# Kernel optimization log

Hardware: AMD Instinct MI355X
Metric: run time of the kernel (lower is better)

The kernel has to match this reference:

```python
import jax, jax.numpy as jnp
import numpy as np
import math

B, T, C, H = 8, 1024, 1024, 16
HS = C // H  # head size 64
FF = 4 * C
EPS = 1e-5


def quant_weight(W, e, b):
    """Fake-quant with straight-through rounding, per QLinear.forward.
    W:[...,out,in], e:[...,out,1], b:[...,out,1] -> effective weight 2**e * round_ste(clip(2**-e * W))."""
    b_rel = jax.nn.relu(b)
    mn = jnp.where(b_rel > 0, -(2.0 ** (b_rel - 1)), 0.0)
    mx = jnp.where(b_rel > 0, 2.0 ** (b_rel - 1) - 1.0, 0.0)
    qw = jnp.clip((2.0 ** (-e)) * W, mn, mx)
    w = qw + jax.lax.stop_gradient(jnp.round(qw) - qw)  # STE round
    return (2.0 ** e) * w


def layer_norm(x, g, beta):
    mu = jnp.mean(x, axis=-1, keepdims=True)
    var = jnp.mean((x - mu) ** 2, axis=-1, keepdims=True)
    return (x - mu) * jax.lax.rsqrt(var + EPS) * g + beta


def _uniform(key, shape, fan_in):
    s = 1.0 / math.sqrt(fan_in)
    return jax.random.uniform(key, shape, jnp.float32, -s, s)


def setup_inputs() -> dict:
    key = jax.random.key(0)
    ks = jax.random.split(key, 8)
    d = {"x": jax.random.normal(ks[0], (B, T, C), jnp.float32)}
    # stacked per-head QKV QLinear params (bias=False)
    d["Wq"] = _uniform(ks[1], (H, HS, C), C)
    d["Wk"] = _uniform(ks[2], (H, HS, C), C)
    d["Wv"] = _uniform(ks[3], (H, HS, C), C)
    for n in ("q", "k", "v"):
        d["e" + n] = jnp.full((H, HS, 1), -8.0, jnp.float32)
        d["b" + n] = jnp.full((H, HS, 1), 32.0, jnp.float32)
    # output projection QLinear (bias=True)
    d["Wp"] = _uniform(ks[4], (C, C), C)
    d["ep"] = jnp.full((C, 1), -8.0, jnp.float32)
    d["bp"] = jnp.full((C, 1), 32.0, jnp.float32)
    d["biasp"] = jnp.zeros((C,), jnp.float32)
    # FFN QLinears
    d["W1"] = _uniform(ks[5], (FF, C), C)
    d["e1"] = jnp.full((FF, 1), -8.0, jnp.float32)
    d["b1"] = jnp.full((FF, 1), 32.0, jnp.float32)
    d["bias1"] = jnp.zeros((FF,), jnp.float32)
    d["W2"] = _uniform(ks[6], (C, FF), FF)
    d["e2"] = jnp.full((C, 1), -8.0, jnp.float32)
    d["b2"] = jnp.full((C, 1), 32.0, jnp.float32)
    d["bias2"] = jnp.zeros((C,), jnp.float32)
    # LayerNorms
    d["g1"] = jnp.ones((C,), jnp.float32)
    d["be1"] = jnp.zeros((C,), jnp.float32)
    d["g2"] = jnp.ones((C,), jnp.float32)
    d["be2"] = jnp.zeros((C,), jnp.float32)
    return d


def block_forward(x, Wq, eq, bq, Wk, ek, bk, Wv, ev, bv,
                  Wp, ep, bp, biasp, W1, e1, b1, bias1, W2, e2, b2, bias2,
                  g1, be1, g2, be2):
    h = layer_norm(x, g1, be1)
    q = jnp.einsum('btc,hdc->bhtd', h, quant_weight(Wq, eq, bq))
    k = jnp.einsum('btc,hdc->bhtd', h, quant_weight(Wk, ek, bk))
    v = jnp.einsum('btc,hdc->bhtd', h, quant_weight(Wv, ev, bv))
    # NOTE: source scales by C**-0.5 where C = n_embd (not head_size)
    wei = jnp.einsum('bhtd,bhsd->bhts', q, k) * (C ** -0.5)
    causal = jnp.tril(jnp.ones((T, T), bool))
    wei = jnp.where(causal, wei, -jnp.inf)
    wei = jax.nn.softmax(wei, axis=-1)
    att = jnp.einsum('bhts,bhsd->bhtd', wei, v)  # [B,H,T,HS]
    att = att.transpose(0, 2, 1, 3).reshape(B, T, C)  # concat heads
    x = x + att @ quant_weight(Wp, ep, bp).T + biasp
    h2 = layer_norm(x, g2, be2)
    f = jax.nn.relu(h2 @ quant_weight(W1, e1, b1).T + bias1)
    f = f @ quant_weight(W2, e2, b2).T + bias2
    return x + f


def reference(x, Wq, eq, bq, Wk, ek, bk, Wv, ev, bv,
              Wp, ep, bp, biasp, W1, e1, b1, bias1, W2, e2, b2, bias2,
              g1, be1, g2, be2):
    return block_forward(x, Wq, eq, bq, Wk, ek, bk, Wv, ev, bv,
                         Wp, ep, bp, biasp, W1, e1, b1, bias1, W2, e2, b2, bias2,
                         g1, be1, g2, be2)
```

## Files before the change

kernel.cpp:

```cpp
#include <hip/hip_runtime.h>
#include <hip/hip_bf16.h>
#include <math.h>

#define DEVI __device__ __forceinline__

typedef __attribute__((ext_vector_type(8))) short bf16x8;
typedef __attribute__((ext_vector_type(4))) float f32x4;

DEVI unsigned short f2bf(float f) {
    union { float f; unsigned u; } v; v.f = f;
    unsigned r = v.u + 0x7FFFu + ((v.u >> 16) & 1u);
    return (unsigned short)(r >> 16);
}

DEVI void gload16(const void* g, void* l) {
    __builtin_amdgcn_global_load_lds((const __attribute__((address_space(1))) void*)g,
                                     (__attribute__((address_space(3))) void*)l, 16, 0, 0);
}

#define WAITVM8() asm volatile("s_waitcnt vmcnt(8)" ::: "memory")
#define WAITVM0() asm volatile("s_waitcnt vmcnt(0)" ::: "memory")
#define WAITLG0() asm volatile("s_waitcnt lgkmcnt(0)" ::: "memory")

__global__ __launch_bounds__(256) void quant6_kernel(
    const float* __restrict__ Wq, const float* __restrict__ Wk, const float* __restrict__ Wv,
    const float* __restrict__ Wp, const float* __restrict__ W1, const float* __restrict__ W2,
    const float* __restrict__ eq, const float* __restrict__ ek, const float* __restrict__ ev,
    const float* __restrict__ ep, const float* __restrict__ e1, const float* __restrict__ e2,
    const float* __restrict__ bq, const float* __restrict__ bk, const float* __restrict__ bv,
    const float* __restrict__ bp, const float* __restrict__ b1, const float* __restrict__ b2,
    unsigned short* __restrict__ Wqkvq, unsigned short* __restrict__ Wpq,
    unsigned short* __restrict__ W1q, unsigned short* __restrict__ W2q)
{
    const int M1 = 1 << 20;
    const int NCH = 3 * M1;
    for (int c = blockIdx.x * blockDim.x + threadIdx.x; c < NCH; c += gridDim.x * blockDim.x) {
        int elem = c * 4;
        const float *W, *e, *b; unsigned short* o; int lgK, local;
        if (elem < M1)            { W = Wq; e = eq; b = bq; o = Wqkvq;          lgK = 10; local = elem; }
        else if (elem < 2 * M1)   { W = Wk; e = ek; b = bk; o = Wqkvq + M1;     lgK = 10; local = elem - M1; }
        else if (elem < 3 * M1)   { W = Wv; e = ev; b = bv; o = Wqkvq + 2 * M1; lgK = 10; local = elem - 2 * M1; }
        else if (elem < 4 * M1)   { W = Wp; e = ep; b = bp; o = Wpq;            lgK = 10; local = elem - 3 * M1; }
        else if (elem < 8 * M1)   { W = W1; e = e1; b = b1; o = W1q;            lgK = 10; local = elem - 4 * M1; }
        else                      { W = W2; e = e2; b = b2; o = W2q;            lgK = 12; local = elem - 8 * M1; }
        int row = local >> lgK;
        float evv = e[row], bvv = b[row];
        float br = fmaxf(bvv, 0.f);
        float mn, mx;
        if (br > 0.f) { float p = exp2f(br - 1.f); mn = -p; mx = p - 1.f; }
        else          { mn = 0.f; mx = 0.f; }
        float si = exp2f(-evv), so = exp2f(evv);
        union { float4 v4; float a[4]; } v;
        v.v4 = *(const float4*)(W + local);
        union { unsigned short u[4]; unsigned long long ll; } ot;
        #pragma unroll
        for (int j = 0; j < 4; j++) {
            float qw = fminf(fmaxf(si * v.a[j], mn), mx);
            ot.u[j] = f2bf(so * rintf(qw));
        }
        *(unsigned long long*)(o + local) = ot.ll;
    }
}

__global__ __launch_bounds__(256) void ln_kernel(
    const float* __restrict__ x, const float* __restrict__ g, const float* __restrict__ be,
    unsigned short* __restrict__ out)
{
    int row = blockIdx.x;
    union { float4 v4; float a[4]; } v;
    v.v4 = ((const float4*)(x + (size_t)row * 1024))[threadIdx.x];
    float s = v.a[0] + v.a[1] + v.a[2] + v.a[3];
    float s2 = v.a[0]*v.a[0] + v.a[1]*v.a[1] + v.a[2]*v.a[2] + v.a[3]*v.a[3];
    #pragma unroll
    for (int off = 32; off > 0; off >>= 1) { s += __shfl_down(s, off); s2 += __shfl_down(s2, off); }
    __shared__ float ps[4], ps2[4];
    int wave = threadIdx.x >> 6, lane = threadIdx.x & 63;
    if (lane == 0) { ps[wave] = s; ps2[wave] = s2; }
    __syncthreads();
    float mu = (ps[0] + ps[1] + ps[2] + ps[3]) * (1.0f / 1024.0f);
    float var = (ps2[0] + ps2[1] + ps2[2] + ps2[3]) * (1.0f / 1024.0f) - mu * mu;
    float rs = rsqrtf(var + 1e-5f);
    int c = threadIdx.x * 4;
    union { unsigned short u[4]; unsigned long long ll; } o;
    #pragma unroll
    for (int j = 0; j < 4; j++) o.u[j] = f2bf((v.a[j] - mu) * rs * g[c + j] + be[c + j]);
    *(unsigned long long*)(out + (size_t)row * 1024 + c) = o.ll;
}

#define GSTAGE(buf, kt) do { \
    _Pragma("unroll") for (int q_ = 0; q_ < 4; q_++) { \
        int idx_ = q_ * 256 + tid; int row_ = idx_ >> 3; int gs_ = (idx_ & 7) ^ (row_ & 7); \
        gload16(A  + (size_t)(brow + row_) * K + (kt) * 64 + gs_ * 8, &As[buf][idx_ * 8]); \
        gload16(Bw + (size_t)(bcol + row_) * K + (kt) * 64 + gs_ * 8, &Bs[buf][idx_ * 8]); \
    } } while (0)

template<int EP>
__global__ __launch_bounds__(256) void gemm_bt(
    const unsigned short* __restrict__ A, const unsigned short* __restrict__ Bw,
    int N, int K,
    const float* __restrict__ bias, const float* __restrict__ res,
    float* __restrict__ outf, unsigned short* __restrict__ outb)
{
    __shared__ __align__(16) unsigned short As[2][128 * 64];
    __shared__ __align__(16) unsigned short Bs[2][128 * 64];
    int tid = threadIdx.x, lane = tid & 63, wave = tid >> 6;
    int gx = gridDim.x;
    int nwg = gx * gridDim.y;
    int id = blockIdx.y * gx + blockIdx.x;
    int swz = (id & 7) * (nwg >> 3) + (id >> 3);
    int brow = (swz / gx) * 128, bcol = (swz % gx) * 128;
    int wr = wave >> 1, wc = wave & 1;
    int r = lane & 15, g4 = lane >> 4;
    f32x4 acc[4][4];
    #pragma unroll
    for (int i = 0; i < 4; i++)
        #pragma unroll
        for (int j = 0; j < 4; j++) acc[i][j] = (f32x4){0.f, 0.f, 0.f, 0.f};

    int nt = K >> 6;
    GSTAGE(0, 0);
    __syncthreads();
    int cur = 0;
    for (int t = 0; t < nt; ++t) {
        if (t + 1 < nt) { GSTAGE(cur ^ 1, t + 1); WAITVM8(); }
        else            { WAITVM0(); }
        __builtin_amdgcn_s_barrier();
        #pragma unroll
        for (int kk = 0; kk < 2; kk++) {
            bf16x8 af[4], bfr[4];
            #pragma unroll
            for (int mi = 0; mi < 4; mi++) {
                int rh = wr * 64 + mi * 16 + r;
                af[mi] = *(const bf16x8*)&As[cur][rh * 64 + (((kk * 4 + g4) ^ (rh & 7)) << 3)];
            }
            #pragma unroll
            for (int ni = 0; ni < 4; ni++) {
                int rh = wc * 64 + ni * 16 + r;
                bfr[ni] = *(const bf16x8*)&Bs[cur][rh * 64 + (((kk * 4 + g4) ^ (rh & 7)) << 3)];
            }
            #pragma unroll
            for (int mi = 0; mi < 4; mi++)
                #pragma unroll
                for (int ni = 0; ni < 4; ni++)
                    acc[mi][ni] = __builtin_amdgcn_mfma_f32_16x16x32_bf16(af[mi], bfr[ni], acc[mi][ni], 0, 0, 0);
        }
        __builtin_amdgcn_s_barrier();
        cur ^= 1;
    }

    #pragma unroll
    for (int mi = 0; mi < 4; mi++)
        #pragma unroll
        for (int ni = 0; ni < 4; ni++)
            #pragma unroll
            for (int i = 0; i < 4; i++) {
                int row = brow + wr * 64 + mi * 16 + g4 * 4 + i;
                int col = bcol + wc * 64 + ni * 16 + r;
                float v = acc[mi][ni][i];
                if (EP == 0) {
                    outb[(size_t)row * N + col] = f2bf(v);
                } else if (EP == 1) {
                    outf[(size_t)row * N + col] = v + bias[col] + res[(size_t)row * N + col];
                } else {
                    outb[(size_t)row * N + col] = f2bf(fmaxf(v + bias[col], 0.f));
                }
            }
}

__global__ __launch_bounds__(256) void attn_kernel(
    const unsigned short* __restrict__ qkv, unsigned short* __restrict__ att)
{
    __shared__ __align__(16) unsigned short Ks[2][64 * 64];
    __shared__ __align__(16) unsigned short Vt[2][64 * 64];
    __shared__ __align__(16) unsigned short Ps[64 * 64];
    int tid = threadIdx.x, lane = tid & 63, wave = tid >> 6;
    int pi = blockIdx.x;
    int bh = blockIdx.y, bb = bh >> 4, hh = bh & 15;
    int r = lane & 15, g4 = lane >> 4;
    const unsigned short* base = qkv + (size_t)bb * 1024 * 3072;
    const float SCL = 0.03125f * 1.4426950408889634f;
    int vd = tid & 63, vsb = tid >> 6;
    int prow = wave * 16 + r;
    int pswz = (r & 7) << 3;

    #pragma unroll
    for (int sub = 0; sub < 2; sub++) {
        int qi = sub ? (15 - pi) : pi;
        int q0 = qi * 64;
        int qrow = q0 + prow;

        bf16x8 qf[2];
        #pragma unroll
        for (int kk = 0; kk < 2; kk++)
            qf[kk] = *(const bf16x8*)&base[(size_t)qrow * 3072 + hh * 64 + kk * 32 + g4 * 8];

        f32x4 oacc[4];
        #pragma unroll
        for (int i = 0; i < 4; i++) oacc[i] = (f32x4){0.f, 0.f, 0.f, 0.f};
        float m_i = -INFINITY, l_i = 0.f;

        unsigned short vtmp[16];
        {
            #pragma unroll
            for (int half = 0; half < 2; half++) {
                int idx = half * 256 + tid;
                int row = idx >> 3, slot = idx & 7;
                int gs = slot ^ (row & 7);
                gload16(base + (size_t)row * 3072 + 1024 + hh * 64 + gs * 8, &Ks[0][idx * 8]);
            }
            #pragma unroll
            for (int i2 = 0; i2 < 16; i2++)
                vtmp[i2] = base[(size_t)(vsb * 16 + i2) * 3072 + 2048 + hh * 64 + vd];
            union { unsigned short u[8]; bf16x8 v; } w0, w1;
            #pragma unroll
            for (int i2 = 0; i2 < 8; i2++) { w0.u[i2] = vtmp[i2]; w1.u[i2] = vtmp[8 + i2]; }
            int s0 = (vsb * 2) ^ (vd & 7), s1 = (vsb * 2 + 1) ^ (vd & 7);
            *(bf16x8*)&Vt[0][vd * 64 + s0 * 8] = w0.v;
            *(bf16x8*)&Vt[0][vd * 64 + s1 * 8] = w1.v;
        }
        __syncthreads();

        for (int ki = 0; ki <= qi; ki++) {
            int cur = ki & 1;
            bool pre = (ki < qi);
            if (pre) {
                int k1 = (ki + 1) * 64;
                #pragma unroll
                for (int half = 0; half < 2; half++) {
                    int idx = half * 256 + tid;
                    int row = idx >> 3, slot = idx & 7;
                    int gs = slot ^ (row & 7);
                    gload16(base + (size_t)(k1 + row) * 3072 + 1024 + hh * 64 + gs * 8, &Ks[cur ^ 1][idx * 8]);
                }
                #pragma unroll
                for (int i2 = 0; i2 < 16; i2++)
                    vtmp[i2] = base[(size_t)(k1 + vsb * 16 + i2) * 3072 + 2048 + hh * 64 + vd];
            }

            int k0 = ki * 64;
            f32x4 sacc[4];
            #pragma unroll
            for (int c4 = 0; c4 < 4; c4++) sacc[c4] = (f32x4){0.f, 0.f, 0.f, 0.f};
            #pragma unroll
            for (int c4 = 0; c4 < 4; c4++) {
                int krow = c4 * 16 + r;
                #pragma unroll
                for (int kk = 0; kk < 2; kk++) {
                    int slot = (g4 + kk * 4) ^ (krow & 7);
                    bf16x8 kf = *(const bf16x8*)&Ks[cur][krow * 64 + slot * 8];
                    sacc[c4] = __builtin_amdgcn_mfma_f32_16x16x32_bf16(kf, qf[kk], sacc[c4], 0, 0, 0);
                }
            }
            bool diag = (ki == qi);
            float sv[4][4];
            float smax = -INFINITY;
            #pragma unroll
            for (int c4 = 0; c4 < 4; c4++)
                #pragma unroll
                for (int i = 0; i < 4; i++) {
                    float s = sacc[c4][i];
                    if (diag && (k0 + c4 * 16 + g4 * 4 + i) > qrow) s = -INFINITY;
                    sv[c4][i] = s;
                    smax = fmaxf(smax, s);
                }
            smax = fmaxf(smax, __shfl_xor(smax, 16));
            smax = fmaxf(smax, __shfl_xor(smax, 32));
            float mn = fmaxf(m_i, smax);
            float fs = exp2f((m_i - mn) * SCL);
            float nb = -mn * SCL;
            m_i = mn;
            float rsum = 0.f;
            float pv[4][4];
            #pragma unroll
            for (int c4 = 0; c4 < 4; c4++)
                #pragma unroll
                for (int i = 0; i < 4; i++) {
                    float p = exp2f(fmaf(sv[c4][i], SCL, nb));
                    pv[c4][i] = p;
                    rsum += p;
                }
            rsum += __shfl_xor(rsum, 16);
            rsum += __shfl_xor(rsum, 32);
            l_i = l_i * fs + rsum;
            #pragma unroll
            for (int n4 = 0; n4 < 4; n4++)
                #pragma unroll
                for (int i = 0; i < 4; i++) oacc[n4][i] *= fs;
            #pragma unroll
            for (int c4 = 0; c4 < 4; c4++) {
                union { unsigned short u[4]; unsigned long long ll; } pk;
                #pragma unroll
                for (int i = 0; i < 4; i++) pk.u[i] = f2bf(pv[c4][i]);
                int idx16 = (prow * 64 + c4 * 16 + g4 * 4) ^ pswz;
                *(unsigned long long*)&Ps[idx16] = pk.ll;
            }
            WAITLG0();
            if (pre) {
                union { unsigned short u[8]; bf16x8 v; } w0, w1;
                #pragma unroll
                for (int i2 = 0; i2 < 8; i2++) { w0.u[i2] = vtmp[i2]; w1.u[i2] = vtmp[8 + i2]; }
                int s0 = (vsb * 2) ^ (vd & 7), s1 = (vsb * 2 + 1) ^ (vd & 7);
                *(bf16x8*)&Vt[cur ^ 1][vd * 64 + s0 * 8] = w0.v;
                *(bf16x8*)&Vt[cur ^ 1][vd * 64 + s1 * 8] = w1.v;
            }
            bf16x8 pa[2];
            #pragma unroll
            for (int kk = 0; kk < 2; kk++)
                pa[kk] = *(const bf16x8*)&Ps[(prow * 64 + kk * 32 + g4 * 8) ^ pswz];
            #pragma unroll
            for (int n4 = 0; n4 < 4; n4++) {
                int d = n4 * 16 + r;
                #pragma unroll
                for (int kk = 0; kk < 2; kk++) {
                    bf16x8 vf = *(const bf16x8*)&Vt[cur][d * 64 + (((kk * 4 + g4) ^ (d & 7)) << 3)];
                    oacc[n4] = __builtin_amdgcn_mfma_f32_16x16x32_bf16(vf, pa[kk], oacc[n4], 0, 0, 0);
                }
            }
            __syncthreads();
        }

        float inv = 1.f / l_i;
        #pragma unroll
        for (int n4 = 0; n4 < 4; n4++) {
            union { unsigned short u[4]; unsigned long long ll; } ok;
            #pragma unroll
            for (int i = 0; i < 4; i++) ok.u[i] = f2bf(oacc[n4][i] * inv);
            size_t oidx = ((size_t)(bb * 1024 + qrow)) * 1024 + hh * 64 + n4 * 16 + g4 * 4;
            *(unsigned long long*)&att[oidx] = ok.ll;
        }
    }
}

extern "C" void kernel_launch(void* const* d_in, const int* in_sizes, int n_in,
                              void* d_out, int out_size, void* d_ws, size_t ws_size,
                              hipStream_t stream)
{
    const float* x     = (const float*)d_in[0];
    const float* Wq    = (const float*)d_in[1];
    const float* Wk    = (const float*)d_in[2];
    const float* Wv    = (const float*)d_in[3];
    const float* eq    = (const float*)d_in[4];
    const float* bq    = (const float*)d_in[5];
    const float* ek    = (const float*)d_in[6];
    const float* bk    = (const float*)d_in[7];
    const float* ev    = (const float*)d_in[8];
    const float* bv    = (const float*)d_in[9];
    const float* Wp    = (const float*)d_in[10];
    const float* ep    = (const float*)d_in[11];
    const float* bp    = (const float*)d_in[12];
    const float* biasp = (const float*)d_in[13];
    const float* W1    = (const float*)d_in[14];
    const float* e1    = (const float*)d_in[15];
    const float* b1    = (const float*)d_in[16];
    const float* bias1 = (const float*)d_in[17];
    const float* W2    = (const float*)d_in[18];
    const float* e2    = (const float*)d_in[19];
    const float* b2    = (const float*)d_in[20];
    const float* bias2 = (const float*)d_in[21];
    const float* g1    = (const float*)d_in[22];
    const float* be1   = (const float*)d_in[23];
    const float* g2    = (const float*)d_in[24];
    const float* be2   = (const float*)d_in[25];

    const size_t MB = 1ull << 20;
    char* ws = (char*)d_ws;
    unsigned short* Wqkvq = (unsigned short*)(ws);
    unsigned short* Wpq   = (unsigned short*)(ws + 6 * MB);
    unsigned short* W1q   = (unsigned short*)(ws + 8 * MB);
    unsigned short* W2q   = (unsigned short*)(ws + 16 * MB);
    unsigned short* hbuf  = (unsigned short*)(ws + 24 * MB);
    unsigned short* qkvb  = (unsigned short*)(ws + 40 * MB);
    unsigned short* fbuf  = qkvb;
    unsigned short* attb  = (unsigned short*)(ws + 88 * MB);
    float*          x2    = (float*)(ws + 104 * MB);

    quant6_kernel<<<2048, 256, 0, stream>>>(Wq, Wk, Wv, Wp, W1, W2,
                                            eq, ek, ev, ep, e1, e2,
                                            bq, bk, bv, bp, b1, b2,
                                            Wqkvq, Wpq, W1q, W2q);

    ln_kernel<<<8192, 256, 0, stream>>>(x, g1, be1, hbuf);
    gemm_bt<0><<<dim3(24, 64), 256, 0, stream>>>(hbuf, Wqkvq, 3072, 1024, nullptr, nullptr, nullptr, qkvb);
    attn_kernel<<<dim3(8, 128), 256, 0, stream>>>(qkvb, attb);
    gemm_bt<1><<<dim3(8, 64), 256, 0, stream>>>(attb, Wpq, 1024, 1024, biasp, x, x2, nullptr);
    ln_kernel<<<8192, 256, 0, stream>>>(x2, g2, be2, hbuf);
    gemm_bt<2><<<dim3(32, 64), 256, 0, stream>>>(hbuf, W1q, 4096, 1024, bias1, nullptr, nullptr, fbuf);
    gemm_bt<1><<<dim3(8, 64), 256, 0, stream>>>(fbuf, W2q, 1024, 4096, bias2, x2, (float*)d_out, nullptr);
}
```

Measured before the change: 356.7 us.

## Add 256x256 ping-pong GEMM kernel for QKV and FFN1 projections

New measurement: 349.5 us. 1.02x faster.

```diff
diff --git a/kernel.cpp b/kernel.cpp
--- a/kernel.cpp
+++ b/kernel.cpp
@@ -19,8 +19,12 @@
 }
 
 #define WAITVM8() asm volatile("s_waitcnt vmcnt(8)" ::: "memory")
+#define WAITVM4() asm volatile("s_waitcnt vmcnt(4)" ::: "memory")
 #define WAITVM0() asm volatile("s_waitcnt vmcnt(0)" ::: "memory")
 #define WAITLG0() asm volatile("s_waitcnt lgkmcnt(0)" ::: "memory")
+#define WAITLG8() asm volatile("s_waitcnt lgkmcnt(8)" ::: "memory")
+#define BAR()     __builtin_amdgcn_s_barrier()
+#define SB()      __builtin_amdgcn_sched_barrier(0)
 
 __global__ __launch_bounds__(256) void quant6_kernel(
     const float* __restrict__ Wq, const float* __restrict__ Wk, const float* __restrict__ Wv,
@@ -167,6 +171,137 @@
             }
 }
 
+#define STAGE_A(b, h, kt) do { \
+    _Pragma("unroll") \
+    for (int ld = 0; ld < 2; ld++) { \
+        int idx = ld * 512 + tid; int rw = idx >> 3; int gs = (idx & 7) ^ (rw & 7); \
+        gload16(Aa + (size_t)(brow + (h) * 128 + rw) * K + (kt) * 64 + gs * 8, &As[b][h][idx * 8]); \
+    } } while (0)
+
+#define STAGE_B(b, h, kt) do { \
+    _Pragma("unroll") \
+    for (int ld = 0; ld < 2; ld++) { \
+        int idx = ld * 512 + tid; int rw = idx >> 3; int gs = (idx & 7) ^ (rw & 7); \
+        gload16(Bw + (size_t)(bcol + (h) * 128 + rw) * K + (kt) * 64 + gs * 8, &Bs[b][h][idx * 8]); \
+    } } while (0)
+
+#define RD_A(b, mh) do { \
+    _Pragma("unroll") for (int mi = 0; mi < 4; mi++) \
+    _Pragma("unroll") for (int kk = 0; kk < 2; kk++) { \
+        int rh = (mh) * 64 + mi * 16 + r; \
+        af[mi][kk] = *(const bf16x8*)&As[b][wr][rh * 64 + (((kk * 4 + g4) ^ (rh & 7)) << 3)]; \
+    } } while (0)
+
+#define RD_B2(b, nh) do { \
+    _Pragma("unroll") for (int nj = 0; nj < 2; nj++) \
+    _Pragma("unroll") for (int kk = 0; kk < 2; kk++) { \
+        int rh = (wc & 1) * 64 + ((nh) * 2 + nj) * 16 + r; \
+        bfr[(nh) * 2 + nj][kk] = *(const bf16x8*)&Bs[b][wc >> 1][rh * 64 + (((kk * 4 + g4) ^ (rh & 7)) << 3)]; \
+    } } while (0)
+
+#define QUAD(mh, nh) do { \
+    __builtin_amdgcn_s_setprio(1); \
+    _Pragma("unroll") for (int mi = 0; mi < 4; mi++) \
+    _Pragma("unroll") for (int nj = 0; nj < 2; nj++) \
+    _Pragma("unroll") for (int kk = 0; kk < 2; kk++) \
+        acc[(mh) * 4 + mi][(nh) * 2 + nj] = __builtin_amdgcn_mfma_f32_16x16x32_bf16( \
+            af[mi][kk], bfr[(nh) * 2 + nj][kk], acc[(mh) * 4 + mi][(nh) * 2 + nj], 0, 0, 0); \
+    __builtin_amdgcn_s_setprio(0); \
+    } while (0)
+
+template<int EP>
+__global__ __launch_bounds__(512, 2) void gemm256(
+    const unsigned short* __restrict__ Aa, const unsigned short* __restrict__ Bw,
+    int N, int K,
+    const float* __restrict__ bias, const float* __restrict__ res,
+    float* __restrict__ outf, unsigned short* __restrict__ outb)
+{
+    __shared__ __align__(16) unsigned short As[2][2][128 * 64];
+    __shared__ __align__(16) unsigned short Bs[2][2][128 * 64];
+    int tid = threadIdx.x, lane = tid & 63, wave = tid >> 6;
+    int gx = gridDim.x;
+    int nwg = gx * gridDim.y;
+    int id = blockIdx.y * gx + blockIdx.x;
+    int swz = (id & 7) * (nwg >> 3) + (id >> 3);
+    int brow = (swz / gx) * 256, bcol = (swz % gx) * 256;
+    int wr = wave >> 2, wc = wave & 3;
+    int r = lane & 15, g4 = lane >> 4;
+    int KT = K >> 6;
+
+    f32x4 acc[8][4];
+    #pragma unroll
+    for (int i = 0; i < 8; i++)
+        #pragma unroll
+        for (int j = 0; j < 4; j++) acc[i][j] = (f32x4){0.f, 0.f, 0.f, 0.f};
+    bf16x8 af[4][2], bfr[4][2];
+
+    STAGE_A(0, 0, 0); STAGE_A(0, 1, 0); STAGE_B(0, 0, 0); STAGE_B(0, 1, 0);
+    STAGE_B(1, 0, 1); STAGE_B(1, 1, 1);
+    WAITVM4();
+    BAR();
+
+    for (int t = 0; t < KT; t += 2) {
+        RD_A(0, 0); RD_B2(0, 0);
+        STAGE_A(1, 0, t + 1);
+        WAITLG8();
+        BAR(); WAITLG0(); SB();
+        QUAD(0, 0);
+        BAR();
+        RD_B2(0, 1);
+        STAGE_A(1, 1, t + 1);
+        BAR(); WAITLG0(); SB();
+        QUAD(0, 1);
+        BAR();
+        RD_A(0, 1);
+        if (t + 2 < KT) STAGE_B(0, 0, t + 2);
+        BAR(); WAITLG0(); SB();
+        QUAD(1, 1);
+        BAR();
+        if (t + 2 < KT) { STAGE_B(0, 1, t + 2); WAITVM4(); } else { WAITVM0(); }
+        BAR(); WAITLG0(); SB();
+        QUAD(1, 0);
+        BAR();
+        RD_A(1, 0); RD_B2(1, 0);
+        if (t + 2 < KT) STAGE_A(0, 0, t + 2);
+        WAITLG8();
+        BAR(); WAITLG0(); SB();
+        QUAD(0, 0);
+        BAR();
+        RD_B2(1, 1);
+        if (t + 2 < KT) STAGE_A(0, 1, t + 2);
+        BAR(); WAITLG0(); SB();
+        QUAD(0, 1);
+        BAR();
+        RD_A(1, 1);
+        if (t + 3 < KT) STAGE_B(1, 0, t + 3);
+        BAR(); WAITLG0(); SB();
+        QUAD(1, 1);
+        BAR();
+        if (t + 3 < KT) { STAGE_B(1, 1, t + 3); WAITVM4(); } else { WAITVM0(); }
+        BAR(); WAITLG0(); SB();
+        QUAD(1, 0);
+        BAR();
+    }
+
+    #pragma unroll
+    for (int m = 0; m < 8; m++)
+        #pragma unroll
+        for (int n = 0; n < 4; n++)
+            #pragma unroll
+            for (int j = 0; j < 4; j++) {
+                int row = brow + wr * 128 + m * 16 + g4 * 4 + j;
+                int col = bcol + wc * 64 + n * 16 + r;
+                float v = acc[m][n][j];
+                if (EP == 0) {
+                    outb[(size_t)row * N + col] = f2bf(v);
+                } else if (EP == 1) {
+                    outf[(size_t)row * N + col] = v + bias[col] + res[(size_t)row * N + col];
+                } else {
+                    outb[(size_t)row * N + col] = f2bf(fmaxf(v + bias[col], 0.f));
+                }
+            }
+}
+
 __global__ __launch_bounds__(256) void attn_kernel(
     const unsigned short* __restrict__ qkv, unsigned short* __restrict__ att)
 {
@@ -380,10 +515,10 @@
                                             Wqkvq, Wpq, W1q, W2q);
 
     ln_kernel<<<8192, 256, 0, stream>>>(x, g1, be1, hbuf);
-    gemm_bt<0><<<dim3(24, 64), 256, 0, stream>>>(hbuf, Wqkvq, 3072, 1024, nullptr, nullptr, nullptr, qkvb);
+    gemm256<0><<<dim3(12, 32), 512, 0, stream>>>(hbuf, Wqkvq, 3072, 1024, nullptr, nullptr, nullptr, qkvb);
     attn_kernel<<<dim3(8, 128), 256, 0, stream>>>(qkvb, attb);
     gemm_bt<1><<<dim3(8, 64), 256, 0, stream>>>(attb, Wpq, 1024, 1024, biasp, x, x2, nullptr);
     ln_kernel<<<8192, 256, 0, stream>>>(x2, g2, be2, hbuf);
-    gemm_bt<2><<<dim3(32, 64), 256, 0, stream>>>(hbuf, W1q, 4096, 1024, bias1, nullptr, nullptr, fbuf);
+    gemm256<2><<<dim3(16, 32), 512, 0, stream>>>(hbuf, W1q, 4096, 1024, bias1, nullptr, nullptr, fbuf);
     gemm_bt<1><<<dim3(8, 64), 256, 0, stream>>>(fbuf, W2q, 1024, 4096, bias2, x2, (float*)d_out, nullptr);
 }
```
